# Optimization experiments

Measured on AMD Instinct MI355X. Metric: run time of the kernel, lower is better.

## Reference

```python
import jax, jax.numpy as jnp
import numpy as np

B, N, D = 4, 2048, 512
H, DA, DL = 8, 64, 64  # heads, attention_dim, linear_dim
EPS = 1e-6


def _layer_norm(x, eps=EPS):
    # F.layer_norm with no affine params
    mu = jnp.mean(x, axis=-1, keepdims=True)
    var = jnp.var(x, axis=-1, keepdims=True)
    return (x - mu) * jax.lax.rsqrt(var + eps)


def setup_inputs() -> dict:
    key = jax.random.key(0)
    k1, k2, k3, k4 = jax.random.split(key, 4)
    x = jax.random.normal(k1, (B, N, D), dtype=jnp.float32)
    # causal (lower-triangular) valid-attention mask, float {0,1}, shape (B,1,N,N)
    attention_mask = jnp.broadcast_to(
        jnp.tril(jnp.ones((N, N), dtype=jnp.float32))[None, None], (B, 1, N, N)
    )
    # _uvqk: (D, 2*H*DL + 2*H*DA), init normal(0, 0.02)
    uvqk = 0.02 * jax.random.normal(k2, (D, 2 * H * DL + 2 * H * DA), dtype=jnp.float32)
    # _o: Linear(H*DL -> D), xavier uniform
    fan_in, fan_out = H * DL, D
    limit = float(np.sqrt(6.0 / (fan_in + fan_out)))
    o_weight = jax.random.uniform(k3, (fan_out, fan_in), dtype=jnp.float32, minval=-limit, maxval=limit)
    o_bias = jnp.zeros((D,), dtype=jnp.float32)
    return {"x": x, "attention_mask": attention_mask, "uvqk": uvqk,
            "o_weight": o_weight, "o_bias": o_bias}


def reference(x, attention_mask, uvqk, o_weight, o_bias):
    b, n, _ = x.shape
    normed_x = _layer_norm(x)
    mm = jax.nn.silu(normed_x @ uvqk)  # fused uvqk projection + silu
    u, v, q, k = jnp.split(mm, [H * DL, 2 * H * DL, 2 * H * DL + H * DA], axis=-1)
    qh = q.reshape(b, n, H, DA)
    kh = k.reshape(b, n, H, DA)
    vh = v.reshape(b, n, H, DL)
    # silu-activated (non-softmax) attention with mask
    qk = jnp.einsum('bnhd,bmhd->bhnm', qh, kh)
    qk = jax.nn.silu(qk) / n
    qk = qk * attention_mask  # (B,1,N,N) broadcast over heads
    attn = jnp.einsum('bhnm,bmhd->bnhd', qk, vh).reshape(b, n, H * DL)
    # gated norm + output proj + residual
    o_input = u * _layer_norm(attn)
    return o_input @ o_weight.T + o_bias + x
```

## Files before the change

### kernel.cpp

```cpp
#include <hip/hip_runtime.h>

typedef __bf16 bf16x8 __attribute__((ext_vector_type(8)));
typedef float f32x4 __attribute__((ext_vector_type(4)));
typedef float f32x16 __attribute__((ext_vector_type(16)));

__device__ __forceinline__ unsigned short f2bf(float f) {
  return __builtin_bit_cast(unsigned short, (__bf16)f);
}
__device__ __forceinline__ float bfu2f(unsigned short b) {
  unsigned int u = ((unsigned int)b) << 16;
  return __builtin_bit_cast(float, u);
}
__device__ __forceinline__ float silu_f(float x) {
  return x * __builtin_amdgcn_rcpf(1.0f + __expf(-x));
}
__device__ __forceinline__ unsigned pk2(float a, float b) {
  return (unsigned)f2bf(a) | ((unsigned)f2bf(b) << 16);
}

template<int CPR, int NI, int SWZ>
__device__ __forceinline__ void stage16(const __bf16* __restrict__ g, int ld,
                                        __bf16* lds, int wave, int lane) {
#pragma unroll
  for (int t = 0; t < NI; ++t) {
    int cb = (wave * NI + t) * 64;
    int c = cb + lane;
    int row = c / CPR;
    int colb = (c % CPR) ^ (row & SWZ);
    __builtin_amdgcn_global_load_lds(
        (const __attribute__((address_space(1))) unsigned int*)(g + row * ld + colb * 8),
        (__attribute__((address_space(3))) unsigned int*)(lds + cb * 8),
        16, 0, 0);
  }
}

__global__ void k_prep(const float* __restrict__ x, __bf16* __restrict__ nx,
                       const float* __restrict__ ow, __bf16* __restrict__ owb,
                       const float* __restrict__ uvqk, __bf16* __restrict__ uvqkT) {
  int bid = blockIdx.x, tid = threadIdx.x;
  if (bid < 4096) {
    int t = tid & 127;
    int r = bid * 2 + (tid >> 7);
    int wave = tid >> 6;
    float4 v = ((const float4*)(x + (size_t)r * 512))[t];
    float s = v.x + v.y + v.z + v.w;
    float ss = v.x * v.x + v.y * v.y + v.z * v.z + v.w * v.w;
#pragma unroll
    for (int o = 32; o > 0; o >>= 1) { s += __shfl_down(s, o); ss += __shfl_down(ss, o); }
    __shared__ float red[4][2];
    if ((tid & 63) == 0) { red[wave][0] = s; red[wave][1] = ss; }
    __syncthreads();
    int rw = (wave >> 1) * 2;
    s = red[rw][0] + red[rw + 1][0];
    ss = red[rw][1] + red[rw + 1][1];
    float mu = s * (1.0f / 512.0f);
    float var = ss * (1.0f / 512.0f) - mu * mu;
    float rs = rsqrtf(var + 1e-6f);
    ushort4 o4;
    o4.x = f2bf((v.x - mu) * rs); o4.y = f2bf((v.y - mu) * rs);
    o4.z = f2bf((v.z - mu) * rs); o4.w = f2bf((v.w - mu) * rs);
    ((ushort4*)(nx + (size_t)r * 512))[t] = o4;
  } else if (bid < 4352) {
    int i = (bid - 4096) * 256 + tid;
    float4 v = ((const float4*)ow)[i];
    ushort4 o4;
    o4.x = f2bf(v.x); o4.y = f2bf(v.y); o4.z = f2bf(v.z); o4.w = f2bf(v.w);
    ((ushort4*)owb)[i] = o4;
  } else {
    __shared__ float tile[32][33];
    int bb = bid - 4352;
    int n0 = (bb & 63) * 32, k0 = (bb >> 6) * 32;
    int tx = tid & 31, ty = tid >> 5;
    for (int i = ty; i < 32; i += 8)
      tile[i][tx] = uvqk[(k0 + i) * 2048 + n0 + tx];
    __syncthreads();
    for (int i = ty; i < 32; i += 8)
      uvqkT[(n0 + i) * 512 + k0 + tx] = (__bf16)tile[tx][i];
  }
}

__global__ __launch_bounds__(256, 2) void k_proj(
    const __bf16* __restrict__ A, const __bf16* __restrict__ Bt,
    __bf16* __restrict__ u, __bf16* __restrict__ qn,
    __bf16* __restrict__ kn, __bf16* __restrict__ vt) {
  __shared__ __bf16 As[128 * 64];
  __shared__ __bf16 Bs[256 * 64];
  int tid = threadIdx.x, wave = tid >> 6, lane = tid & 63;
  int lr = lane & 15, lq = lane >> 4;
  int bn = blockIdx.x, bm = blockIdx.y;
  const __bf16* Ag = A + (size_t)bm * 128 * 512;
  const __bf16* Bg = Bt + (size_t)bn * 256 * 512;
  int wm = (wave >> 1) * 64, wn2 = (wave & 1) * 128;
  f32x4 acc[4][8] = {};
  for (int k0 = 0; k0 < 512; k0 += 64) {
    stage16<8, 4, 7>(Ag + k0, 512, As, wave, lane);
    stage16<8, 8, 7>(Bg + k0, 512, Bs, wave, lane);
    __syncthreads();
#pragma unroll
    for (int kk = 0; kk < 2; ++kk) {
      int b = kk * 4 + lq;
      bf16x8 a[4], bb[8];
#pragma unroll
      for (int i = 0; i < 4; ++i) {
        int row = wm + i * 16 + lr;
        a[i] = *(const bf16x8*)(As + row * 64 + ((b ^ (row & 7)) * 8));
      }
#pragma unroll
      for (int j = 0; j < 8; ++j) {
        int row = wn2 + j * 16 + lr;
        bb[j] = *(const bf16x8*)(Bs + row * 64 + ((b ^ (row & 7)) * 8));
      }
#pragma unroll
      for (int i = 0; i < 4; ++i)
#pragma unroll
        for (int j = 0; j < 8; ++j)
          acc[i][j] = __builtin_amdgcn_mfma_f32_16x16x32_bf16(a[i], bb[j], acc[i][j], 0, 0, 0);
    }
    __syncthreads();
  }
  int seg = bn >> 1;
  int cb = (bn & 1) * 256 + wn2;
  int rb0 = bm * 128 + wm + lq * 4;
  if (seg == 1) {
#pragma unroll
    for (int i = 0; i < 4; ++i) {
      int rb = rb0 + i * 16;
      int b = rb >> 11, n = rb & 2047;
#pragma unroll
      for (int j = 0; j < 8; ++j) {
        int c = cb + j * 16 + lr;
        ushort4 w;
        w.x = f2bf(silu_f(acc[i][j][0]) * (1.0f / 2048.0f));
        w.y = f2bf(silu_f(acc[i][j][1]) * (1.0f / 2048.0f));
        w.z = f2bf(silu_f(acc[i][j][2]) * (1.0f / 2048.0f));
        w.w = f2bf(silu_f(acc[i][j][3]) * (1.0f / 2048.0f));
        *(ushort4*)(vt + ((size_t)(b * 512 + c)) * 2048 + n) = w;
      }
    }
  } else {
    __bf16* dst = (seg == 0) ? u : ((seg == 2) ? qn : kn);
#pragma unroll
    for (int i = 0; i < 4; ++i) {
      int rb = rb0 + i * 16;
#pragma unroll
      for (int j = 0; j < 8; ++j) {
        int c = cb + j * 16 + lr;
#pragma unroll
        for (int rg = 0; rg < 4; ++rg)
          dst[(size_t)(rb + rg) * 512 + c] = (__bf16)silu_f(acc[i][j][rg]);
      }
    }
  }
}

__global__ __launch_bounds__(256, 4) void k_attn(
    const __bf16* __restrict__ qn, const __bf16* __restrict__ kn,
    const __bf16* __restrict__ vt, __bf16* __restrict__ oa,
    __bf16* __restrict__ ob) {
  __shared__ __bf16 lds[20480];
  __bf16* Qs = lds;
  __bf16* Kb0 = lds + 4096;
  __bf16* Kb1 = lds + 8192;
  __bf16* Vb0 = lds + 12288;
  __bf16* Vb1 = lds + 16384;

  int bh = blockIdx.x, p = blockIdx.y, z = blockIdx.z;
  int b = bh >> 3, hd = bh & 7;
  int tid = threadIdx.x, wave = tid >> 6, lane = tid & 63;
  int l31 = lane & 31, lh = lane >> 5;
  int wm = (wave >> 1) * 32, wn = (wave & 1) * 32;
  const __bf16* Kg = kn + (size_t)(b * 2048) * 512 + hd * 64;
  const __bf16* Vg = vt + (size_t)(b * 512 + hd * 64) * 2048;
  __bf16* Oz = z ? ob : oa;

  for (int ph = 0; ph < 2; ++ph) {
    int t = ph ? (31 - p) : p;
    int c0 = (t + 2) >> 1;
    int mlo = z ? c0 : 0;
    int cnt = (z ? (t + 1) : c0) - mlo;
    const __bf16* Qg = qn + (size_t)(b * 2048 + t * 64) * 512 + hd * 64;
    if (ph) __syncthreads();
    stage16<8, 2, 7>(Qg, 512, Qs, wave, lane);
    if (cnt > 0) {
      stage16<8, 2, 7>(Kg + (size_t)mlo * 64 * 512, 512, Kb0, wave, lane);
      stage16<8, 2, 7>(Vg + mlo * 64, 2048, Vb0, wave, lane);
    }
    __syncthreads();

    bf16x8 qf[4];
#pragma unroll
    for (int ks = 0; ks < 4; ++ks) {
      int row = wn + l31;
      qf[ks] = *(const bf16x8*)(Qs + row * 64 + (((ks * 2 + lh) ^ (row & 7)) * 8));
    }

    f32x16 po[2] = {};

    for (int i = 0; i < cnt; ++i) {
      int mt = mlo + i;
      const __bf16* Kc = (i & 1) ? Kb1 : Kb0;
      const __bf16* Vc = (i & 1) ? Vb1 : Vb0;
      if (i + 1 < cnt) {
        __bf16* Kn_ = (i & 1) ? Kb0 : Kb1;
        __bf16* Vn_ = (i & 1) ? Vb0 : Vb1;
        stage16<8, 2, 7>(Kg + (size_t)(mt + 1) * 64 * 512, 512, Kn_, wave, lane);
        stage16<8, 2, 7>(Vg + (mt + 1) * 64, 2048, Vn_, wave, lane);
      }
      f32x16 s = {};
#pragma unroll
      for (int ks = 0; ks < 4; ++ks) {
        int row = wm + l31;
        bf16x8 ak = *(const bf16x8*)(Kc + row * 64 + (((ks * 2 + lh) ^ (row & 7)) * 8));
        s = __builtin_amdgcn_mfma_f32_32x32x16_bf16(ak, qf[ks], s, 0, 0, 0);
      }
      bool diag = (mt == t);
      bool full = diag && (wm > wn + 31);
      bool dtile = diag && !full && (wm + 31 > wn);
      unsigned pk[8];
      if (full) {
#pragma unroll
        for (int q = 0; q < 8; ++q) pk[q] = 0u;
      } else {
        float vv[16];
#pragma unroll
        for (int r = 0; r < 16; ++r) {
          float xx = s[r];
          float pv = xx * __builtin_amdgcn_rcpf(1.0f + __expf(-xx));
          if (dtile) {
            int mrow = wm + 4 * lh + (r & 3) + 8 * (r >> 2);
            int ncol = wn + l31;
            if (mrow > ncol) pv = 0.0f;
          }
          vv[r] = pv;
        }
#pragma unroll
        for (int q = 0; q < 8; ++q) pk[q] = pk2(vv[2 * q], vv[2 * q + 1]);
      }
      bool lo = (lh == 0);
      unsigned xa = __shfl_xor(lo ? pk[2] : pk[0], 32);
      unsigned xb = __shfl_xor(lo ? pk[3] : pk[1], 32);
      unsigned xc = __shfl_xor(lo ? pk[6] : pk[4], 32);
      unsigned xd = __shfl_xor(lo ? pk[7] : pk[5], 32);
      union { bf16x8 v; unsigned u[4]; } f0, f1;
      f0.u[0] = lo ? pk[0] : xa;  f0.u[1] = lo ? pk[1] : xb;
      f0.u[2] = lo ? xa : pk[2];  f0.u[3] = lo ? xb : pk[3];
      f1.u[0] = lo ? pk[4] : xc;  f1.u[1] = lo ? pk[5] : xd;
      f1.u[2] = lo ? xc : pk[6];  f1.u[3] = lo ? xd : pk[7];
      bf16x8 pf[2] = { f0.v, f1.v };
#pragma unroll
      for (int t2 = 0; t2 < 2; ++t2) {
#pragma unroll
        for (int idl = 0; idl < 2; ++idl) {
          int row = idl * 32 + l31;
          bf16x8 av = *(const bf16x8*)(Vc + row * 64 +
              ((((wm >> 3) + t2 * 2 + lh) ^ (row & 7)) * 8));
          po[idl] = __builtin_amdgcn_mfma_f32_32x32x16_bf16(av, pf[t2], po[idl], 0, 0, 0);
        }
      }
      __syncthreads();
    }

    float* red = (float*)(Kb0);
    __bf16* bo = Vb1;
    if (wave >= 2) {
      float* dst = red + (wave - 2) * 2048;
#pragma unroll
      for (int idl = 0; idl < 2; ++idl)
#pragma unroll
        for (int r = 0; r < 16; ++r)
          dst[(idl * 16 + r) * 64 + lane] = po[idl][r];
    }
    __syncthreads();
    if (wave < 2) {
      float* src = red + wave * 2048;
      int nrow = wn + l31;
#pragma unroll
      for (int idl = 0; idl < 2; ++idl) {
#pragma unroll
        for (int r = 0; r < 16; ++r)
          po[idl][r] += src[(idl * 16 + r) * 64 + lane];
#pragma unroll
        for (int g = 0; g < 4; ++g) {
          int dl0 = idl * 32 + g * 8 + lh * 4;
          int addr = nrow * 64 + ((((dl0 >> 3) ^ (nrow & 7)) << 3) | (dl0 & 7));
          ushort4 w;
          w.x = f2bf(po[idl][4 * g + 0]); w.y = f2bf(po[idl][4 * g + 1]);
          w.z = f2bf(po[idl][4 * g + 2]); w.w = f2bf(po[idl][4 * g + 3]);
          *(ushort4*)(bo + addr) = w;
        }
      }
    }
    __syncthreads();
    {
      int n = tid >> 2, cc = (tid & 3) * 16;
      __bf16* gdst = Oz + (size_t)(b * 2048 + t * 64 + n) * 512 + hd * 64 + cc;
      int a0 = n * 64 + (((cc >> 3) ^ (n & 7)) << 3);
      int a1 = n * 64 + ((((cc >> 3) + 1) ^ (n & 7)) << 3);
      *(uint4*)(gdst) = *(const uint4*)(bo + a0);
      *(uint4*)(gdst + 8) = *(const uint4*)(bo + a1);
    }
  }
}

__global__ void k_oinput(const __bf16* __restrict__ oa, const __bf16* __restrict__ ob,
                         const __bf16* __restrict__ u, __bf16* __restrict__ oin) {
  int r = blockIdx.x, t = threadIdx.x;
  ushort4 a4 = ((const ushort4*)(oa + (size_t)r * 512))[t];
  ushort4 b4 = ((const ushort4*)(ob + (size_t)r * 512))[t];
  float a0 = bfu2f(a4.x) + bfu2f(b4.x), a1 = bfu2f(a4.y) + bfu2f(b4.y);
  float a2 = bfu2f(a4.z) + bfu2f(b4.z), a3 = bfu2f(a4.w) + bfu2f(b4.w);
  float s = a0 + a1 + a2 + a3;
  float ss = a0 * a0 + a1 * a1 + a2 * a2 + a3 * a3;
#pragma unroll
  for (int o = 32; o > 0; o >>= 1) { s += __shfl_down(s, o); ss += __shfl_down(ss, o); }
  __shared__ float red[4];
  if ((t & 63) == 0) { red[(t >> 6) * 2] = s; red[(t >> 6) * 2 + 1] = ss; }
  __syncthreads();
  s = red[0] + red[2]; ss = red[1] + red[3];
  float mu = s * (1.0f / 512.0f);
  float var = ss * (1.0f / 512.0f) - mu * mu;
  float rs = rsqrtf(var + 1e-6f);
  ushort4 u4 = ((const ushort4*)(u + (size_t)r * 512))[t];
  ushort4 o4;
  o4.x = f2bf(bfu2f(u4.x) * (a0 - mu) * rs);
  o4.y = f2bf(bfu2f(u4.y) * (a1 - mu) * rs);
  o4.z = f2bf(bfu2f(u4.z) * (a2 - mu) * rs);
  o4.w = f2bf(bfu2f(u4.w) * (a3 - mu) * rs);
  ((ushort4*)(oin + (size_t)r * 512))[t] = o4;
}

__global__ __launch_bounds__(256, 4) void k_out(
    const __bf16* __restrict__ A, const __bf16* __restrict__ Bt,
    const float* __restrict__ bias, const float* __restrict__ x,
    float* __restrict__ out) {
  __shared__ __bf16 As[64 * 64];
  __shared__ __bf16 Bs[128 * 64];
  int tid = threadIdx.x, wave = tid >> 6, lane = tid & 63;
  int lr = lane & 15, lq = lane >> 4;
  int bn = blockIdx.x, bm = blockIdx.y;
  const __bf16* Ag = A + (size_t)bm * 64 * 512;
  const __bf16* Bg = Bt + (size_t)bn * 128 * 512;
  int wm = (wave >> 1) * 32, wn = (wave & 1) * 64;
  f32x4 acc[2][4] = {};
  for (int k0 = 0; k0 < 512; k0 += 64) {
    stage16<8, 2, 7>(Ag + k0, 512, As, wave, lane);
    stage16<8, 4, 7>(Bg + k0, 512, Bs, wave, lane);
    __syncthreads();
#pragma unroll
    for (int kk = 0; kk < 2; ++kk) {
      int b = kk * 4 + lq;
      bf16x8 a[2], bb[4];
#pragma unroll
      for (int i = 0; i < 2; ++i) {
        int row = wm + i * 16 + lr;
        a[i] = *(const bf16x8*)(As + row * 64 + ((b ^ (row & 7)) * 8));
      }
#pragma unroll
      for (int j = 0; j < 4; ++j) {
        int row = wn + j * 16 + lr;
        bb[j] = *(const bf16x8*)(Bs + row * 64 + ((b ^ (row & 7)) * 8));
      }
#pragma unroll
      for (int i = 0; i < 2; ++i)
#pragma unroll
        for (int j = 0; j < 4; ++j)
          acc[i][j] = __builtin_amdgcn_mfma_f32_16x16x32_bf16(a[i], bb[j], acc[i][j], 0, 0, 0);
    }
    __syncthreads();
  }
  int cb = bn * 128 + wn;
  int rb0 = bm * 64 + wm + lq * 4;
#pragma unroll
  for (int j = 0; j < 4; ++j) {
    int c = cb + j * 16 + lr;
    float bv = bias[c];
#pragma unroll
    for (int i = 0; i < 2; ++i) {
      int rb = rb0 + i * 16;
#pragma unroll
      for (int rg = 0; rg < 4; ++rg) {
        size_t idx = (size_t)(rb + rg) * 512 + c;
        out[idx] = acc[i][j][rg] + bv + x[idx];
      }
    }
  }
}

extern "C" void kernel_launch(void* const* d_in, const int* in_sizes, int n_in,
                              void* d_out, int out_size, void* d_ws, size_t ws_size,
                              hipStream_t stream) {
  const float* x = (const float*)d_in[0];
  const float* uvqk = (const float*)d_in[2];
  const float* ow = (const float*)d_in[3];
  const float* obias = (const float*)d_in[4];
  float* out = (float*)d_out;

  char* w = (char*)d_ws;
  const size_t MB8 = 8u * 1024 * 1024;
  __bf16* nx    = (__bf16*)(w);
  __bf16* u     = (__bf16*)(w + MB8);
  __bf16* qn    = (__bf16*)(w + 2 * MB8);
  __bf16* kn    = (__bf16*)(w + 3 * MB8);
  __bf16* vt    = (__bf16*)(w + 4 * MB8);
  __bf16* uvqkT = (__bf16*)(w + 5 * MB8);
  __bf16* owb   = (__bf16*)(w + 5 * MB8 + 2097152);
  __bf16* Oa    = nx;
  __bf16* Ob    = (__bf16*)d_out;
  __bf16* o_in  = qn;

  k_prep<<<5376, 256, 0, stream>>>(x, nx, ow, owb, uvqk, uvqkT);
  k_proj<<<dim3(8, 64), 256, 0, stream>>>(nx, uvqkT, u, qn, kn, vt);
  k_attn<<<dim3(32, 16, 2), 256, 0, stream>>>(qn, kn, vt, Oa, Ob);
  k_oinput<<<8192, 128, 0, stream>>>(Oa, Ob, u, o_in);
  k_out<<<dim3(4, 128), 256, 0, stream>>>(o_in, owb, obias, x, out);
}
```

Measured before the change: 196.8 us.

## Use 128-row query tiles per wave with three-way key split

Each attention block now covers 128 query rows, with each wave owning 32 of them and holding its Q fragments in registers loaded straight from global memory. The Q staging buffer and the cross-wave reduction through LDS are gone. Every K/V tile loaded into LDS is now reused by four times as many query rows. The causal key range is split three ways across the z dimension instead of two, which adds a third partial output buffer that k_oinput must also read and sum. This cuts K/V traffic and removes the reduction sync, at the cost of extra partial-output memory and coarser, possibly less balanced work units.

```diff
diff --git a/kernel.cpp b/kernel.cpp
--- a/kernel.cpp
+++ b/kernel.cpp
@@ -156,43 +156,38 @@
 __global__ __launch_bounds__(256, 4) void k_attn(
     const __bf16* __restrict__ qn, const __bf16* __restrict__ kn,
     const __bf16* __restrict__ vt, __bf16* __restrict__ oa,
-    __bf16* __restrict__ ob) {
-  __shared__ __bf16 lds[20480];
-  __bf16* Qs = lds;
-  __bf16* Kb0 = lds + 4096;
-  __bf16* Kb1 = lds + 8192;
-  __bf16* Vb0 = lds + 12288;
-  __bf16* Vb1 = lds + 16384;
+    __bf16* __restrict__ ob, __bf16* __restrict__ oc) {
+  __shared__ __bf16 lds[16384];
+  __bf16* Kb0 = lds;
+  __bf16* Kb1 = lds + 4096;
+  __bf16* Vb0 = lds + 8192;
+  __bf16* Vb1 = lds + 12288;
+  __bf16* bo = lds;
 
   int bh = blockIdx.x, p = blockIdx.y, z = blockIdx.z;
   int b = bh >> 3, hd = bh & 7;
   int tid = threadIdx.x, wave = tid >> 6, lane = tid & 63;
   int l31 = lane & 31, lh = lane >> 5;
-  int wm = (wave >> 1) * 32, wn = (wave & 1) * 32;
   const __bf16* Kg = kn + (size_t)(b * 2048) * 512 + hd * 64;
   const __bf16* Vg = vt + (size_t)(b * 512 + hd * 64) * 2048;
-  __bf16* Oz = z ? ob : oa;
+  __bf16* Oz = (z == 0) ? oa : ((z == 1) ? ob : oc);
 
   for (int ph = 0; ph < 2; ++ph) {
-    int t = ph ? (31 - p) : p;
-    int c0 = (t + 2) >> 1;
-    int mlo = z ? c0 : 0;
-    int cnt = (z ? (t + 1) : c0) - mlo;
-    const __bf16* Qg = qn + (size_t)(b * 2048 + t * 64) * 512 + hd * 64;
+    int t = ph ? (15 - p) : p;
+    int T = 2 * t + 2;
+    int mlo = z * T / 3;
+    int cnt = (z + 1) * T / 3 - mlo;
+    int n0 = t * 128 + wave * 32;
     if (ph) __syncthreads();
-    stage16<8, 2, 7>(Qg, 512, Qs, wave, lane);
+    const __bf16* Qg = qn + (size_t)(b * 2048 + n0 + l31) * 512 + hd * 64 + lh * 8;
+    bf16x8 qf[4];
+#pragma unroll
+    for (int ks = 0; ks < 4; ++ks) qf[ks] = *(const bf16x8*)(Qg + ks * 16);
     if (cnt > 0) {
       stage16<8, 2, 7>(Kg + (size_t)mlo * 64 * 512, 512, Kb0, wave, lane);
       stage16<8, 2, 7>(Vg + mlo * 64, 2048, Vb0, wave, lane);
     }
     __syncthreads();
-
-    bf16x8 qf[4];
-#pragma unroll
-    for (int ks = 0; ks < 4; ++ks) {
-      int row = wn + l31;
-      qf[ks] = *(const bf16x8*)(Qs + row * 64 + (((ks * 2 + lh) ^ (row & 7)) * 8));
-    }
 
     f32x16 po[2] = {};
 
@@ -206,79 +201,62 @@
         stage16<8, 2, 7>(Kg + (size_t)(mt + 1) * 64 * 512, 512, Kn_, wave, lane);
         stage16<8, 2, 7>(Vg + (mt + 1) * 64, 2048, Vn_, wave, lane);
       }
-      f32x16 s = {};
-#pragma unroll
-      for (int ks = 0; ks < 4; ++ks) {
-        int row = wm + l31;
-        bf16x8 ak = *(const bf16x8*)(Kc + row * 64 + (((ks * 2 + lh) ^ (row & 7)) * 8));
-        s = __builtin_amdgcn_mfma_f32_32x32x16_bf16(ak, qf[ks], s, 0, 0, 0);
-      }
-      bool diag = (mt == t);
-      bool full = diag && (wm > wn + 31);
-      bool dtile = diag && !full && (wm + 31 > wn);
-      unsigned pk[8];
-      if (full) {
-#pragma unroll
-        for (int q = 0; q < 8; ++q) pk[q] = 0u;
-      } else {
+#pragma unroll
+      for (int ms = 0; ms < 2; ++ms) {
+        int m0 = mt * 64 + ms * 32;
+        if (m0 > n0 + 31) continue;
+        f32x16 s = {};
+#pragma unroll
+        for (int ks = 0; ks < 4; ++ks) {
+          int row = ms * 32 + l31;
+          bf16x8 ak = *(const bf16x8*)(Kc + row * 64 + (((ks * 2 + lh) ^ (row & 7)) * 8));
+          s = __builtin_amdgcn_mfma_f32_32x32x16_bf16(ak, qf[ks], s, 0, 0, 0);
+        }
+        bool dtile = (m0 + 31 > n0);
         float vv[16];
 #pragma unroll
         for (int r = 0; r < 16; ++r) {
           float xx = s[r];
           float pv = xx * __builtin_amdgcn_rcpf(1.0f + __expf(-xx));
           if (dtile) {
-            int mrow = wm + 4 * lh + (r & 3) + 8 * (r >> 2);
-            int ncol = wn + l31;
+            int mrow = m0 + 4 * lh + (r & 3) + 8 * (r >> 2);
+            int ncol = n0 + l31;
             if (mrow > ncol) pv = 0.0f;
           }
           vv[r] = pv;
         }
+        unsigned pk[8];
 #pragma unroll
         for (int q = 0; q < 8; ++q) pk[q] = pk2(vv[2 * q], vv[2 * q + 1]);
-      }
-      bool lo = (lh == 0);
-      unsigned xa = __shfl_xor(lo ? pk[2] : pk[0], 32);
-      unsigned xb = __shfl_xor(lo ? pk[3] : pk[1], 32);
-      unsigned xc = __shfl_xor(lo ? pk[6] : pk[4], 32);
-      unsigned xd = __shfl_xor(lo ? pk[7] : pk[5], 32);
-      union { bf16x8 v; unsigned u[4]; } f0, f1;
-      f0.u[0] = lo ? pk[0] : xa;  f0.u[1] = lo ? pk[1] : xb;
-      f0.u[2] = lo ? xa : pk[2];  f0.u[3] = lo ? xb : pk[3];
-      f1.u[0] = lo ? pk[4] : xc;  f1.u[1] = lo ? pk[5] : xd;
-      f1.u[2] = lo ? xc : pk[6];  f1.u[3] = lo ? xd : pk[7];
-      bf16x8 pf[2] = { f0.v, f1.v };
-#pragma unroll
-      for (int t2 = 0; t2 < 2; ++t2) {
-#pragma unroll
-        for (int idl = 0; idl < 2; ++idl) {
-          int row = idl * 32 + l31;
-          bf16x8 av = *(const bf16x8*)(Vc + row * 64 +
-              ((((wm >> 3) + t2 * 2 + lh) ^ (row & 7)) * 8));
-          po[idl] = __builtin_amdgcn_mfma_f32_32x32x16_bf16(av, pf[t2], po[idl], 0, 0, 0);
+        bool lo_ = (lh == 0);
+        unsigned xa = __shfl_xor(lo_ ? pk[2] : pk[0], 32);
+        unsigned xb = __shfl_xor(lo_ ? pk[3] : pk[1], 32);
+        unsigned xc = __shfl_xor(lo_ ? pk[6] : pk[4], 32);
+        unsigned xd = __shfl_xor(lo_ ? pk[7] : pk[5], 32);
+        union { bf16x8 v; unsigned u[4]; } f0, f1;
+        f0.u[0] = lo_ ? pk[0] : xa;  f0.u[1] = lo_ ? pk[1] : xb;
+        f0.u[2] = lo_ ? xa : pk[2];  f0.u[3] = lo_ ? xb : pk[3];
+        f1.u[0] = lo_ ? pk[4] : xc;  f1.u[1] = lo_ ? pk[5] : xd;
+        f1.u[2] = lo_ ? xc : pk[6];  f1.u[3] = lo_ ? xd : pk[7];
+        bf16x8 pf[2] = { f0.v, f1.v };
+#pragma unroll
+        for (int t2 = 0; t2 < 2; ++t2) {
+#pragma unroll
+          for (int idl = 0; idl < 2; ++idl) {
+            int row = idl * 32 + l31;
+            bf16x8 av = *(const bf16x8*)(Vc + row * 64 +
+                (((ms * 4 + t2 * 2 + lh) ^ (row & 7)) * 8));
+            po[idl] = __builtin_amdgcn_mfma_f32_32x32x16_bf16(av, pf[t2], po[idl], 0, 0, 0);
+          }
         }
       }
       __syncthreads();
     }
 
-    float* red = (float*)(Kb0);
-    __bf16* bo = Vb1;
-    if (wave >= 2) {
-      float* dst = red + (wave - 2) * 2048;
-#pragma unroll
-      for (int idl = 0; idl < 2; ++idl)
-#pragma unroll
-        for (int r = 0; r < 16; ++r)
-          dst[(idl * 16 + r) * 64 + lane] = po[idl][r];
-    }
-    __syncthreads();
-    if (wave < 2) {
-      float* src = red + wave * 2048;
-      int nrow = wn + l31;
+    {
+      int nrow = wave * 32 + l31;
 #pragma unroll
       for (int idl = 0; idl < 2; ++idl) {
-#pragma unroll
-        for (int r = 0; r < 16; ++r)
-          po[idl][r] += src[(idl * 16 + r) * 64 + lane];
 #pragma unroll
         for (int g = 0; g < 4; ++g) {
           int dl0 = idl * 32 + g * 8 + lh * 4;
@@ -292,23 +270,29 @@
     }
     __syncthreads();
     {
-      int n = tid >> 2, cc = (tid & 3) * 16;
-      __bf16* gdst = Oz + (size_t)(b * 2048 + t * 64 + n) * 512 + hd * 64 + cc;
-      int a0 = n * 64 + (((cc >> 3) ^ (n & 7)) << 3);
-      int a1 = n * 64 + ((((cc >> 3) + 1) ^ (n & 7)) << 3);
-      *(uint4*)(gdst) = *(const uint4*)(bo + a0);
-      *(uint4*)(gdst + 8) = *(const uint4*)(bo + a1);
+      int n = tid >> 1, cc = (tid & 1) * 32;
+      __bf16* gdst = Oz + (size_t)(b * 2048 + t * 128 + n) * 512 + hd * 64 + cc;
+#pragma unroll
+      for (int kk2 = 0; kk2 < 4; ++kk2) {
+        int dlb = cc + kk2 * 8;
+        int a = n * 64 + (((dlb >> 3) ^ (n & 7)) << 3);
+        *(uint4*)(gdst + kk2 * 8) = *(const uint4*)(bo + a);
+      }
     }
   }
 }
 
 __global__ void k_oinput(const __bf16* __restrict__ oa, const __bf16* __restrict__ ob,
-                         const __bf16* __restrict__ u, __bf16* __restrict__ oin) {
+                         const __bf16* __restrict__ oc, const __bf16* __restrict__ u,
+                         __bf16* __restrict__ oin) {
   int r = blockIdx.x, t = threadIdx.x;
   ushort4 a4 = ((const ushort4*)(oa + (size_t)r * 512))[t];
   ushort4 b4 = ((const ushort4*)(ob + (size_t)r * 512))[t];
-  float a0 = bfu2f(a4.x) + bfu2f(b4.x), a1 = bfu2f(a4.y) + bfu2f(b4.y);
-  float a2 = bfu2f(a4.z) + bfu2f(b4.z), a3 = bfu2f(a4.w) + bfu2f(b4.w);
+  ushort4 c4 = ((const ushort4*)(oc + (size_t)r * 512))[t];
+  float a0 = bfu2f(a4.x) + bfu2f(b4.x) + bfu2f(c4.x);
+  float a1 = bfu2f(a4.y) + bfu2f(b4.y) + bfu2f(c4.y);
+  float a2 = bfu2f(a4.z) + bfu2f(b4.z) + bfu2f(c4.z);
+  float a3 = bfu2f(a4.w) + bfu2f(b4.w) + bfu2f(c4.w);
   float s = a0 + a1 + a2 + a3;
   float ss = a0 * a0 + a1 * a1 + a2 * a2 + a3 * a3;
 #pragma unroll
@@ -406,11 +390,12 @@
   __bf16* owb   = (__bf16*)(w + 5 * MB8 + 2097152);
   __bf16* Oa    = nx;
   __bf16* Ob    = (__bf16*)d_out;
+  __bf16* Oc    = (__bf16*)d_out + (size_t)8192 * 512;
   __bf16* o_in  = qn;
 
   k_prep<<<5376, 256, 0, stream>>>(x, nx, ow, owb, uvqk, uvqkT);
   k_proj<<<dim3(8, 64), 256, 0, stream>>>(nx, uvqkT, u, qn, kn, vt);
-  k_attn<<<dim3(32, 16, 2), 256, 0, stream>>>(qn, kn, vt, Oa, Ob);
-  k_oinput<<<8192, 128, 0, stream>>>(Oa, Ob, u, o_in);
+  k_attn<<<dim3(32, 8, 3), 256, 0, stream>>>(qn, kn, vt, Oa, Ob, Oc);
+  k_oinput<<<8192, 128, 0, stream>>>(Oa, Ob, Oc, u, o_in);
   k_out<<<dim3(4, 128), 256, 0, stream>>>(o_in, owb, obias, x, out);
 }
```

New measurement: 198.9 us. About the same (+1.1%).
